# Performance work log

Measured on AMD Instinct MI355X. Metric: run time of the kernel, lower is better.

The kernel has to match this reference:

```python
import jax, jax.numpy as jnp
import numpy as np

# Corner ordering matches the original vertex_0..vertex_7 construction:
# 1 -> ceil, 0 -> floor, per (x, y, z) axis.
_CORNER_SIGNS = np.array([
    [1, 1, 1],  # v0 (c,c,c)
    [1, 1, 0],  # v1 (c,c,f)
    [1, 0, 1],  # v2 (c,f,c)
    [0, 1, 1],  # v3 (f,c,c)
    [1, 0, 0],  # v4 (c,f,f)
    [0, 1, 0],  # v5 (f,c,f)
    [0, 0, 1],  # v6 (f,f,c)
    [0, 0, 0],  # v7 (f,f,f)
], dtype=bool)

TABLE_SIZE = 524288   # 2**19
NUM_LEVELS = 16
MIN_RES = 16
MAX_RES = 2048
FEATURE_DIM = 2
N_POINTS = 524288


def _hash_corners(corners, table_size, hash_offset):
    # corners: [N, L, 8, 3] int32; uint32 wraparound multiply as in NGP.
    primes = jnp.array([1, 2654435761, 805459861], dtype=jnp.uint32)
    p = corners.astype(jnp.uint32) * primes
    h = p[..., 0] ^ p[..., 1] ^ p[..., 2]
    h = (h % jnp.uint32(table_size)).astype(jnp.int32)
    return h + hash_offset[None, :, None]  # per-level table offset


def setup_inputs() -> dict:
    key = jax.random.key(0)
    kx, kt = jax.random.split(key)
    x = jax.random.uniform(kx, (N_POINTS, 3), dtype=jnp.float32)
    hash_table = jax.random.uniform(
        kt, (TABLE_SIZE * NUM_LEVELS, FEATURE_DIM), dtype=jnp.float32) * 1e-4
    levels = jnp.arange(NUM_LEVELS)
    growth = jnp.exp((jnp.log(float(MAX_RES)) - jnp.log(float(MIN_RES))) / (NUM_LEVELS - 1))
    scalings = jnp.floor(MIN_RES * growth ** levels).astype(jnp.float32)   # [L]
    hash_offset = (levels * TABLE_SIZE).astype(jnp.int32)                  # [L]
    return {"x": x, "hash_table": hash_table, "scalings": scalings,
            "hash_offset": hash_offset, "table_size": TABLE_SIZE}


def reference(x, hash_table, scalings, hash_offset, table_size):
    # x: [N,3], scalings: [L] -> scaled: [N,L,3]
    scaled = x[:, None, :] * scalings[None, :, None]
    cc = jnp.ceil(scaled)
    ff = jnp.floor(scaled)
    t = scaled - ff  # point_offset, [N,L,3]

    signs = jnp.asarray(_CORNER_SIGNS)
    corners = jnp.where(signs[None, None], cc[:, :, None, :], ff[:, :, None, :]).astype(jnp.int32)  # [N,L,8,3]
    idx = _hash_corners(corners, table_size, hash_offset)  # [N,L,8]
    feats = hash_table[idx]                                # [N,L,8,F] (main gather)

    tx, ty = t[..., 0], t[..., 1]
    # NOTE: original indexes point_offset[..., 3] on a size-3 axis; jax gather
    # clamps out-of-bounds indices, so this equals point_offset[..., 2].
    tz = t[..., 2]
    # Weights equivalent to the original nested interpolation tree
    # (f_03/f_12/f_56/f_47 -> f_0312/f_4756 -> encoded), corner order v0..v7.
    w = jnp.stack([
        tx * ty * tz,                      # v0
        tx * (1 - ty) * tz,                # v1
        (1 - tx) * (1 - ty) * tz,          # v2
        (1 - tx) * ty * tz,                # v3
        tx * ty * (1 - tz),                # v4
        tx * (1 - ty) * (1 - tz),          # v5
        (1 - tx) * (1 - ty) * (1 - tz),    # v6
        (1 - tx) * ty * (1 - tz),          # v7
    ], axis=-1)                            # [N,L,8]

    enc = jnp.einsum('nlcf,nlc->nlf', feats, w)  # [N,L,F]
    n, l, f = enc.shape
    return enc.reshape(n, l * f)
```

## Files before the change

### kernel.cpp

```cpp
#include <hip/hip_runtime.h>
#include <cstdint>
#include <cstddef>


typedef float f32x2 __attribute__((ext_vector_type(2)));
typedef float f32x4 __attribute__((ext_vector_type(4)));

#define NUM_LEVELS 16
#define BLOCK 256

__global__ __launch_bounds__(BLOCK) void hashenc_gather(
    const float* __restrict__ x,
    const float* __restrict__ table,
    const float* __restrict__ scalings,
    const int* __restrict__ hash_offset,
    const int* __restrict__ tsp,
    float* __restrict__ ws,
    int n_points, int bpl)
{
    static const int perm_arr[NUM_LEVELS] =
        {15, 0, 14, 1, 13, 2, 12, 3, 11, 4, 10, 9, 8, 7, 6, 5};

    const int bid   = (int)blockIdx.x;
    const int slot  = bid / bpl;
    const int level = perm_arr[slot];
    const int n     = (bid - slot * bpl) * BLOCK + (int)threadIdx.x;
    if (n >= n_points) return;

    const float    s    = scalings[level];
    const int      off  = hash_offset[level];
    const uint32_t ts   = (uint32_t)tsp[0];
    const bool     pow2 = (ts & (ts - 1u)) == 0u;
    const uint32_t mask = ts - 1u;

    const float px = x[n * 3 + 0];
    const float py = x[n * 3 + 1];
    const float pz = x[n * 3 + 2];

    const float sx = px * s, sy = py * s, sz = pz * s;
    const float fxf = floorf(sx), fyf = floorf(sy), fzf = floorf(sz);
    const float cxf = ceilf(sx),  cyf = ceilf(sy),  czf = ceilf(sz);
    const float tx = sx - fxf, ty = sy - fyf, tz = sz - fzf;

    const uint32_t fxi = (uint32_t)(int)fxf, fyi = (uint32_t)(int)fyf, fzi = (uint32_t)(int)fzf;
    const uint32_t cxi = (uint32_t)(int)cxf, cyi = (uint32_t)(int)cyf, czi = (uint32_t)(int)czf;

    const uint32_t P1 = 2654435761u, P2 = 805459861u;
    const uint32_t hyf = fyi * P1, hyc = cyi * P1;
    const uint32_t hzf = fzi * P2, hzc = czi * P2;

    uint32_t h[8];
    h[0] = cxi ^ hyc ^ hzc;
    h[1] = cxi ^ hyc ^ hzf;
    h[2] = cxi ^ hyf ^ hzc;
    h[3] = fxi ^ hyc ^ hzc;
    h[4] = cxi ^ hyf ^ hzf;
    h[5] = fxi ^ hyc ^ hzf;
    h[6] = fxi ^ hyf ^ hzc;
    h[7] = fxi ^ hyf ^ hzf;

    const f32x2* tb = reinterpret_cast<const f32x2*>(table) + off;

    f32x2 f[8];
#pragma unroll
    for (int c = 0; c < 8; ++c) {
        const uint32_t hm = pow2 ? (h[c] & mask) : (h[c] % ts);
        f[c] = tb[hm];
    }

    const float ux = 1.f - tx, uy = 1.f - ty, uz = 1.f - tz;
    float w[8];
    w[0] = tx * ty * tz;
    w[1] = tx * uy * tz;
    w[2] = ux * uy * tz;
    w[3] = ux * ty * tz;
    w[4] = tx * ty * uz;
    w[5] = tx * uy * uz;
    w[6] = ux * uy * uz;
    w[7] = ux * ty * uz;

    f32x2 acc = {0.f, 0.f};
#pragma unroll
    for (int c = 0; c < 8; ++c) {
        acc.x = fmaf(w[c], f[c].x, acc.x);
        acc.y = fmaf(w[c], f[c].y, acc.y);
    }

    f32x2* wsl = reinterpret_cast<f32x2*>(ws) + (size_t)level * n_points;
    __builtin_nontemporal_store(acc, wsl + n);
}

__global__ __launch_bounds__(BLOCK) void hashenc_transpose(
    const float* __restrict__ ws, float* __restrict__ out, int n_points)
{
    __shared__ f32x2 tile[NUM_LEVELS][BLOCK + 2];

    const int base = (int)blockIdx.x * BLOCK;
    const int t    = (int)threadIdx.x;
    const int n    = base + t;
    const bool full = (base + BLOCK) <= n_points;

    if (full) {
#pragma unroll
        for (int l = 0; l < NUM_LEVELS; ++l)
            tile[l][t] = __builtin_nontemporal_load(
                reinterpret_cast<const f32x2*>(ws) + (size_t)l * n_points + n);
        __syncthreads();

        const int p0 = t >> 3;
        const int j  = t & 7;
        f32x4* o = reinterpret_cast<f32x4*>(out + (size_t)base * (NUM_LEVELS * 2));
#pragma unroll
        for (int i = 0; i < 8; ++i) {
            const int p = i * 32 + p0;
            const f32x2 a = tile[2 * j][p];
            const f32x2 b = tile[2 * j + 1][p];
            f32x4 v;
            v.x = a.x; v.y = a.y; v.z = b.x; v.w = b.y;
            __builtin_nontemporal_store(v, o + i * BLOCK + t);
        }
    } else if (n < n_points) {
        f32x2 v[NUM_LEVELS];
#pragma unroll
        for (int l = 0; l < NUM_LEVELS; ++l)
            v[l] = reinterpret_cast<const f32x2*>(ws)[(size_t)l * n_points + n];
        f32x4* o = reinterpret_cast<f32x4*>(out + (size_t)n * (NUM_LEVELS * 2));
#pragma unroll
        for (int i = 0; i < 8; ++i) {
            f32x4 w;
            w.x = v[2*i].x;   w.y = v[2*i].y;
            w.z = v[2*i+1].x; w.w = v[2*i+1].y;
            __builtin_nontemporal_store(w, o + i);
        }
    }
}

__global__ __launch_bounds__(BLOCK) void hashenc_direct(
    const float* __restrict__ x,
    const float* __restrict__ table,
    const float* __restrict__ scalings,
    const int* __restrict__ hash_offset,
    const int* __restrict__ tsp,
    float* __restrict__ out,
    int n_points)
{
    const int tid = blockIdx.x * BLOCK + (int)threadIdx.x;
    if (tid >= n_points * NUM_LEVELS) return;
    const int n = tid >> 4, l = tid & 15;

    const float s = scalings[l];
    const int off = hash_offset[l];
    const uint32_t ts = (uint32_t)tsp[0];
    const bool pow2 = (ts & (ts - 1u)) == 0u;
    const uint32_t mask = ts - 1u;

    const float sx = x[n*3]*s, sy = x[n*3+1]*s, sz = x[n*3+2]*s;
    const float fxf = floorf(sx), fyf = floorf(sy), fzf = floorf(sz);
    const float tx = sx - fxf, ty = sy - fyf, tz = sz - fzf;
    const uint32_t fxi = (uint32_t)(int)fxf, fyi = (uint32_t)(int)fyf, fzi = (uint32_t)(int)fzf;
    const uint32_t cxi = (uint32_t)(int)ceilf(sx), cyi = (uint32_t)(int)ceilf(sy), czi = (uint32_t)(int)ceilf(sz);
    const uint32_t P1 = 2654435761u, P2 = 805459861u;
    const uint32_t hyf = fyi*P1, hyc = cyi*P1, hzf = fzi*P2, hzc = czi*P2;
    uint32_t h[8] = {cxi^hyc^hzc, cxi^hyc^hzf, cxi^hyf^hzc, fxi^hyc^hzc,
                     cxi^hyf^hzf, fxi^hyc^hzf, fxi^hyf^hzc, fxi^hyf^hzf};
    const f32x2* tb = reinterpret_cast<const f32x2*>(table) + off;
    f32x2 f[8];
#pragma unroll
    for (int c = 0; c < 8; ++c) f[c] = tb[pow2 ? (h[c] & mask) : (h[c] % ts)];
    const float ux = 1.f-tx, uy = 1.f-ty, uz = 1.f-tz;
    float w[8] = {tx*ty*tz, tx*uy*tz, ux*uy*tz, ux*ty*tz,
                  tx*ty*uz, tx*uy*uz, ux*uy*uz, ux*ty*uz};
    f32x2 acc = {0.f, 0.f};
#pragma unroll
    for (int c = 0; c < 8; ++c) {
        acc.x = fmaf(w[c], f[c].x, acc.x);
        acc.y = fmaf(w[c], f[c].y, acc.y);
    }
    __builtin_nontemporal_store(acc, reinterpret_cast<f32x2*>(out) + tid);
}

extern "C" void kernel_launch(void* const* d_in, const int* in_sizes, int n_in,
                              void* d_out, int out_size, void* d_ws, size_t ws_size,
                              hipStream_t stream) {
    const float* x           = (const float*)d_in[0];
    const float* hash_table  = (const float*)d_in[1];
    const float* scalings    = (const float*)d_in[2];
    const int*   hash_offset = (const int*)d_in[3];
    const int*   table_size  = (const int*)d_in[4];
    float*       out         = (float*)d_out;

    const int n_points = in_sizes[0] / 3;
    const int bpl      = (n_points + BLOCK - 1) / BLOCK;
    const size_t ws_needed = (size_t)n_points * NUM_LEVELS * 2 * sizeof(float);

    if (ws_size >= ws_needed) {
        hashenc_gather<<<NUM_LEVELS * bpl, BLOCK, 0, stream>>>(
            x, hash_table, scalings, hash_offset, table_size,
            (float*)d_ws, n_points, bpl);
        hashenc_transpose<<<bpl, BLOCK, 0, stream>>>(
            (const float*)d_ws, out, n_points);
    } else {
        const int total = n_points * NUM_LEVELS;
        hashenc_direct<<<(total + BLOCK - 1) / BLOCK, BLOCK, 0, stream>>>(
            x, hash_table, scalings, hash_offset, table_size, out, n_points);
    }
}
```

Measured before the change: 401.9 us.

## Pair floor/ceil-x corners into 16-byte loads and process two points per thread

The gather kernel now handles two points per thread and restructures the eight corner lookups into four pairs sharing y/z hashes. For each pair it issues one 16-byte load covering the aligned entry pair containing the floor-x hash. When the ceil-x hash falls in the same pair it reuses that data, and otherwise it issues a separate 8-byte load. This aims to cut the number of scattered memory transactions and raise memory-level parallelism per thread, at the cost of more registers, extra select logic, and a non-pow2 fallback path.

```diff
diff --git a/kernel.cpp b/kernel.cpp
--- a/kernel.cpp
+++ b/kernel.cpp
@@ -8,6 +8,8 @@
 
 #define NUM_LEVELS 16
 #define BLOCK 256
+#define PPT 2
+#define CHUNK (BLOCK * PPT)
 
 __global__ __launch_bounds__(BLOCK) void hashenc_gather(
     const float* __restrict__ x,
@@ -24,8 +26,8 @@
     const int bid   = (int)blockIdx.x;
     const int slot  = bid / bpl;
     const int level = perm_arr[slot];
-    const int n     = (bid - slot * bpl) * BLOCK + (int)threadIdx.x;
-    if (n >= n_points) return;
+    const int t     = (int)threadIdx.x;
+    const int nb    = (bid - slot * bpl) * CHUNK + t;
 
     const float    s    = scalings[level];
     const int      off  = hash_offset[level];
@@ -33,61 +35,124 @@
     const bool     pow2 = (ts & (ts - 1u)) == 0u;
     const uint32_t mask = ts - 1u;
 
-    const float px = x[n * 3 + 0];
-    const float py = x[n * 3 + 1];
-    const float pz = x[n * 3 + 2];
-
-    const float sx = px * s, sy = py * s, sz = pz * s;
-    const float fxf = floorf(sx), fyf = floorf(sy), fzf = floorf(sz);
-    const float cxf = ceilf(sx),  cyf = ceilf(sy),  czf = ceilf(sz);
-    const float tx = sx - fxf, ty = sy - fyf, tz = sz - fzf;
-
-    const uint32_t fxi = (uint32_t)(int)fxf, fyi = (uint32_t)(int)fyf, fzi = (uint32_t)(int)fzf;
-    const uint32_t cxi = (uint32_t)(int)cxf, cyi = (uint32_t)(int)cyf, czi = (uint32_t)(int)czf;
-
-    const uint32_t P1 = 2654435761u, P2 = 805459861u;
-    const uint32_t hyf = fyi * P1, hyc = cyi * P1;
-    const uint32_t hzf = fzi * P2, hzc = czi * P2;
-
-    uint32_t h[8];
-    h[0] = cxi ^ hyc ^ hzc;
-    h[1] = cxi ^ hyc ^ hzf;
-    h[2] = cxi ^ hyf ^ hzc;
-    h[3] = fxi ^ hyc ^ hzc;
-    h[4] = cxi ^ hyf ^ hzf;
-    h[5] = fxi ^ hyc ^ hzf;
-    h[6] = fxi ^ hyf ^ hzc;
-    h[7] = fxi ^ hyf ^ hzf;
-
-    const f32x2* tb = reinterpret_cast<const f32x2*>(table) + off;
-
-    f32x2 f[8];
-#pragma unroll
-    for (int c = 0; c < 8; ++c) {
-        const uint32_t hm = pow2 ? (h[c] & mask) : (h[c] % ts);
-        f[c] = tb[hm];
-    }
-
-    const float ux = 1.f - tx, uy = 1.f - ty, uz = 1.f - tz;
-    float w[8];
-    w[0] = tx * ty * tz;
-    w[1] = tx * uy * tz;
-    w[2] = ux * uy * tz;
-    w[3] = ux * ty * tz;
-    w[4] = tx * ty * uz;
-    w[5] = tx * uy * uz;
-    w[6] = ux * uy * uz;
-    w[7] = ux * ty * uz;
-
-    f32x2 acc = {0.f, 0.f};
-#pragma unroll
-    for (int c = 0; c < 8; ++c) {
-        acc.x = fmaf(w[c], f[c].x, acc.x);
-        acc.y = fmaf(w[c], f[c].y, acc.y);
-    }
-
+    const f32x2* tb2 = reinterpret_cast<const f32x2*>(table) + off;
+    const f32x4* tb4 = reinterpret_cast<const f32x4*>(table + (size_t)off * 2);
     f32x2* wsl = reinterpret_cast<f32x2*>(ws) + (size_t)level * n_points;
-    __builtin_nontemporal_store(acc, wsl + n);
+
+    int  n[PPT];
+    bool valid[PPT];
+#pragma unroll
+    for (int p = 0; p < PPT; ++p) {
+        n[p] = nb + p * BLOCK;
+        valid[p] = n[p] < n_points;
+    }
+
+    if (pow2) {
+        uint32_t hf[PPT][4], hc[PPT][4], bf[PPT][4];
+        bool     mg[PPT][4];
+        float    wcw[PPT][4], wfw[PPT][4];
+
+#pragma unroll
+        for (int p = 0; p < PPT; ++p) {
+            const int idx = valid[p] ? n[p] : 0;
+            const float px = x[idx * 3 + 0];
+            const float py = x[idx * 3 + 1];
+            const float pz = x[idx * 3 + 2];
+
+            const float sx = px * s, sy = py * s, sz = pz * s;
+            const float fxf = floorf(sx), fyf = floorf(sy), fzf = floorf(sz);
+            const float tx = sx - fxf, ty = sy - fyf, tz = sz - fzf;
+
+            const uint32_t fxi = (uint32_t)(int)fxf;
+            const uint32_t fyi = (uint32_t)(int)fyf;
+            const uint32_t fzi = (uint32_t)(int)fzf;
+            const uint32_t cxi = (uint32_t)(int)ceilf(sx);
+            const uint32_t cyi = (uint32_t)(int)ceilf(sy);
+            const uint32_t czi = (uint32_t)(int)ceilf(sz);
+
+            const uint32_t P1 = 2654435761u, P2 = 805459861u;
+            const uint32_t hyf = fyi * P1, hyc = cyi * P1;
+            const uint32_t hzf = fzi * P2, hzc = czi * P2;
+
+            const uint32_t A[4] = {hyc ^ hzc, hyc ^ hzf, hyf ^ hzc, hyf ^ hzf};
+#pragma unroll
+            for (int j = 0; j < 4; ++j) {
+                hf[p][j] = (fxi ^ A[j]) & mask;
+                hc[p][j] = (cxi ^ A[j]) & mask;
+                bf[p][j] = hf[p][j] >> 1;
+                mg[p][j] = (hc[p][j] >> 1) == bf[p][j];
+            }
+
+            const float ux = 1.f - tx, uy = 1.f - ty, uz = 1.f - tz;
+            wcw[p][0] = tx * ty * tz;  wfw[p][0] = ux * ty * tz;
+            wcw[p][1] = tx * uy * tz;  wfw[p][1] = tx * uy * uz;
+            wcw[p][2] = ux * uy * tz;  wfw[p][2] = ux * uy * uz;
+            wcw[p][3] = tx * ty * uz;  wfw[p][3] = ux * ty * uz;
+        }
+
+        f32x4 q[PPT][4];
+#pragma unroll
+        for (int p = 0; p < PPT; ++p)
+#pragma unroll
+            for (int j = 0; j < 4; ++j)
+                if (valid[p]) q[p][j] = tb4[bf[p][j]];
+
+        f32x2 el[PPT][4];
+#pragma unroll
+        for (int p = 0; p < PPT; ++p)
+#pragma unroll
+            for (int j = 0; j < 4; ++j) {
+                el[p][j].x = 0.f; el[p][j].y = 0.f;
+                if (valid[p] && !mg[p][j]) el[p][j] = tb2[hc[p][j]];
+            }
+
+#pragma unroll
+        for (int p = 0; p < PPT; ++p) {
+            if (!valid[p]) continue;
+            f32x2 acc = {0.f, 0.f};
+#pragma unroll
+            for (int j = 0; j < 4; ++j) {
+                const f32x2 qlo = {q[p][j].x, q[p][j].y};
+                const f32x2 qhi = {q[p][j].z, q[p][j].w};
+                const f32x2 ef = (hf[p][j] & 1u) ? qhi : qlo;
+                const f32x2 eh = (hc[p][j] & 1u) ? qhi : qlo;
+                const f32x2 ec = mg[p][j] ? eh : el[p][j];
+                acc.x = fmaf(wfw[p][j], ef.x, acc.x);
+                acc.y = fmaf(wfw[p][j], ef.y, acc.y);
+                acc.x = fmaf(wcw[p][j], ec.x, acc.x);
+                acc.y = fmaf(wcw[p][j], ec.y, acc.y);
+            }
+            __builtin_nontemporal_store(acc, wsl + n[p]);
+        }
+    } else {
+#pragma unroll
+        for (int p = 0; p < PPT; ++p) {
+            if (!valid[p]) continue;
+            const float px = x[n[p]*3], py = x[n[p]*3+1], pz = x[n[p]*3+2];
+            const float sx = px*s, sy = py*s, sz = pz*s;
+            const float fxf = floorf(sx), fyf = floorf(sy), fzf = floorf(sz);
+            const float tx = sx-fxf, ty = sy-fyf, tz = sz-fzf;
+            const uint32_t fxi = (uint32_t)(int)fxf, fyi = (uint32_t)(int)fyf, fzi = (uint32_t)(int)fzf;
+            const uint32_t cxi = (uint32_t)(int)ceilf(sx), cyi = (uint32_t)(int)ceilf(sy), czi = (uint32_t)(int)ceilf(sz);
+            const uint32_t P1 = 2654435761u, P2 = 805459861u;
+            const uint32_t hyf = fyi*P1, hyc = cyi*P1, hzf = fzi*P2, hzc = czi*P2;
+            uint32_t h[8] = {cxi^hyc^hzc, cxi^hyc^hzf, cxi^hyf^hzc, fxi^hyc^hzc,
+                             cxi^hyf^hzf, fxi^hyc^hzf, fxi^hyf^hzc, fxi^hyf^hzf};
+            f32x2 f[8];
+#pragma unroll
+            for (int c = 0; c < 8; ++c) f[c] = tb2[h[c] % ts];
+            const float ux = 1.f-tx, uy = 1.f-ty, uz = 1.f-tz;
+            float w[8] = {tx*ty*tz, tx*uy*tz, ux*uy*tz, ux*ty*tz,
+                          tx*ty*uz, tx*uy*uz, ux*uy*uz, ux*ty*uz};
+            f32x2 acc = {0.f, 0.f};
+#pragma unroll
+            for (int c = 0; c < 8; ++c) {
+                acc.x = fmaf(w[c], f[c].x, acc.x);
+                acc.y = fmaf(w[c], f[c].y, acc.y);
+            }
+            __builtin_nontemporal_store(acc, wsl + n[p]);
+        }
+    }
 }
 
 __global__ __launch_bounds__(BLOCK) void hashenc_transpose(
@@ -190,14 +255,15 @@
     float*       out         = (float*)d_out;
 
     const int n_points = in_sizes[0] / 3;
-    const int bpl      = (n_points + BLOCK - 1) / BLOCK;
+    const int bpl      = (n_points + CHUNK - 1) / CHUNK;
     const size_t ws_needed = (size_t)n_points * NUM_LEVELS * 2 * sizeof(float);
 
     if (ws_size >= ws_needed) {
         hashenc_gather<<<NUM_LEVELS * bpl, BLOCK, 0, stream>>>(
             x, hash_table, scalings, hash_offset, table_size,
             (float*)d_ws, n_points, bpl);
-        hashenc_transpose<<<bpl, BLOCK, 0, stream>>>(
+        const int bpt = (n_points + BLOCK - 1) / BLOCK;
+        hashenc_transpose<<<bpt, BLOCK, 0, stream>>>(
             (const float*)d_ws, out, n_points);
     } else {
         const int total = n_points * NUM_LEVELS;
```

New measurement: 352.2 us. -12.4%, faster.
